# Optimization experiments

Hardware: AMD Instinct MI355X
Metric: run time of the kernel (lower is better)

The kernel has to match this reference:

```python
import jax, jax.numpy as jnp
import numpy as np

D_MODEL = 1024
D_STATE = 16
DT_RANK = 64
BATCH = 4
SEQ = 4096


def setup_inputs() -> dict:
    key = jax.random.key(0)
    ks = jax.random.split(key, 6)
    x = jax.random.normal(ks[0], (BATCH, SEQ, D_MODEL), dtype=jnp.float32)
    # torch nn.Linear weights: (out_features, in_features)
    W_xproj = jax.random.normal(ks[1], (DT_RANK + 2 * D_STATE, D_MODEL), dtype=jnp.float32) * (1.0 / np.sqrt(D_MODEL))
    W_dt = jax.random.normal(ks[2], (D_MODEL, DT_RANK), dtype=jnp.float32) * (1.0 / np.sqrt(DT_RANK))
    b_dt = jax.random.normal(ks[3], (D_MODEL,), dtype=jnp.float32) * 0.01
    A_log = jax.random.normal(ks[4], (D_MODEL, D_STATE), dtype=jnp.float32)
    D = jax.random.normal(ks[5], (D_MODEL,), dtype=jnp.float32)
    return {"x": x, "W_xproj": W_xproj, "W_dt": W_dt, "b_dt": b_dt, "A_log": A_log, "D": D}


def _selective_scan(x, delta, A, B, C):
    # x, delta: (b, s, d); B, C: (b, s, n); A: (d, n)
    b, s, d = x.shape
    n = A.shape[1]
    h0 = jnp.zeros((b, d, n), dtype=x.dtype)

    def step(h, inp):
        x_t, dt_t, B_t, C_t = inp  # (b,d), (b,d), (b,n), (b,n)
        dA = jnp.exp(dt_t[:, :, None] * A[None, :, :])        # (b,d,n)
        dB = dt_t[:, :, None] * B_t[:, None, :]               # (b,d,n)
        h = h * dA + x_t[:, :, None] * dB                     # (b,d,n)
        y_t = jnp.einsum('bdn,bn->bd', h, C_t)                # (b,d)
        return h, y_t

    # time-major for scan
    xs = (jnp.swapaxes(x, 0, 1), jnp.swapaxes(delta, 0, 1),
          jnp.swapaxes(B, 0, 1), jnp.swapaxes(C, 0, 1))
    _, ys = jax.lax.scan(step, h0, xs)  # ys: (s, b, d)
    return jnp.swapaxes(ys, 0, 1)


def reference(x, W_xproj, W_dt, b_dt, A_log, D):
    xp = jnp.einsum('bsd,pd->bsp', x, W_xproj)                # (b,s,dt_rank+2n)
    delta = jax.nn.softplus(jnp.einsum('bsr,dr->bsd', xp[..., :DT_RANK], W_dt) + b_dt)
    B = xp[..., DT_RANK:DT_RANK + D_STATE]
    C = xp[..., DT_RANK + D_STATE:]
    A = -jnp.exp(A_log)
    y = _selective_scan(x, delta, A, B, C)
    return y + x * D[None, None, :]
```

## Files before the change

### kernel.cpp

```cpp
#include <hip/hip_runtime.h>
#include <cstddef>

#define D_MODEL 1024
#define D_STATE 16
#define DT_RANK 64
#define BATCH 4
#define SEQ 4096
#define NPROJ 96
#define M_TOTAL (BATCH * SEQ)
#define NCHUNK 64
#define CLEN 64
#define KSPLIT 4
#define KSLICE 256

__device__ __forceinline__ float softplus_fast(float v) {
    return fmaxf(v, 0.0f) + __logf(1.0f + __expf(-fabsf(v)));
}

__global__ __launch_bounds__(256) void proj_part_kernel(const float* __restrict__ x,
                                                        const float* __restrict__ W,
                                                        float* __restrict__ part) {
    __shared__ float xs_t[32][68];
    __shared__ float ws_t[32][100];
    const int tid   = threadIdx.x;
    const int row0  = blockIdx.x * 64;
    const int ks    = blockIdx.y;
    const int kbase = ks * KSLICE;
    const int ty = tid >> 4;
    const int tx = tid & 15;

    float acc[4][6];
#pragma unroll
    for (int i = 0; i < 4; ++i)
#pragma unroll
        for (int j = 0; j < 6; ++j) acc[i][j] = 0.0f;

    for (int k0 = kbase; k0 < kbase + KSLICE; k0 += 32) {
        for (int i = tid; i < 64 * 8; i += 256) {
            int r = i >> 3, c4 = i & 7;
            float4 v = *reinterpret_cast<const float4*>(
                &x[(size_t)(row0 + r) * 1024 + k0 + c4 * 4]);
            xs_t[c4 * 4 + 0][r] = v.x; xs_t[c4 * 4 + 1][r] = v.y;
            xs_t[c4 * 4 + 2][r] = v.z; xs_t[c4 * 4 + 3][r] = v.w;
        }
        for (int i = tid; i < 96 * 8; i += 256) {
            int r = i >> 3, c4 = i & 7;
            float4 v = *reinterpret_cast<const float4*>(
                &W[(size_t)r * 1024 + k0 + c4 * 4]);
            ws_t[c4 * 4 + 0][r] = v.x; ws_t[c4 * 4 + 1][r] = v.y;
            ws_t[c4 * 4 + 2][r] = v.z; ws_t[c4 * 4 + 3][r] = v.w;
        }
        __syncthreads();
#pragma unroll 8
        for (int k = 0; k < 32; ++k) {
            float4 av = *reinterpret_cast<const float4*>(&xs_t[k][ty * 4]);
            float2 b0 = *reinterpret_cast<const float2*>(&ws_t[k][tx * 6]);
            float2 b1 = *reinterpret_cast<const float2*>(&ws_t[k][tx * 6 + 2]);
            float2 b2 = *reinterpret_cast<const float2*>(&ws_t[k][tx * 6 + 4]);
            float a[4] = {av.x, av.y, av.z, av.w};
            float b[6] = {b0.x, b0.y, b1.x, b1.y, b2.x, b2.y};
#pragma unroll
            for (int i = 0; i < 4; ++i)
#pragma unroll
                for (int j = 0; j < 6; ++j) acc[i][j] = fmaf(a[i], b[j], acc[i][j]);
        }
        __syncthreads();
    }
    size_t base = ((size_t)ks * M_TOTAL + row0) * NPROJ;
#pragma unroll
    for (int i = 0; i < 4; ++i) {
        size_t rbase = base + (size_t)(ty * 4 + i) * NPROJ + tx * 6;
#pragma unroll
        for (int j = 0; j < 6; ++j) part[rbase + j] = acc[i][j];
    }
}

__global__ __launch_bounds__(256) void reduce_xp_kernel(const float* __restrict__ part,
                                                        float* __restrict__ xp) {
    const size_t stride4 = (size_t)M_TOTAL * NPROJ / 4;
    size_t i = (size_t)blockIdx.x * 256 + threadIdx.x;
    const float4* p = reinterpret_cast<const float4*>(part);
    float4 a = p[i];
    float4 b = p[i + stride4];
    float4 c = p[i + 2 * stride4];
    float4 d = p[i + 3 * stride4];
    float4 o;
    o.x = (a.x + b.x) + (c.x + d.x);
    o.y = (a.y + b.y) + (c.y + d.y);
    o.z = (a.z + b.z) + (c.z + d.z);
    o.w = (a.w + b.w) + (c.w + d.w);
    reinterpret_cast<float4*>(xp)[i] = o;
}

__global__ __launch_bounds__(256) void delta_kernel(const float* __restrict__ xp,
                                                    const float* __restrict__ Wd,
                                                    const float* __restrict__ b_dt,
                                                    float* __restrict__ delta) {
    __shared__ float as_t[32][132];
    __shared__ float bs_t[32][132];
    const int tid  = threadIdx.x;
    const int row0 = blockIdx.x * 128;
    const int col0 = blockIdx.y * 128;
    const int ty = tid >> 4;
    const int tx = tid & 15;

    float acc[8][8];
#pragma unroll
    for (int i = 0; i < 8; ++i)
#pragma unroll
        for (int j = 0; j < 8; ++j) acc[i][j] = 0.0f;

    for (int k0 = 0; k0 < 64; k0 += 32) {
        for (int i = tid; i < 128 * 8; i += 256) {
            int r = i >> 3, c4 = i & 7;
            float4 v = *reinterpret_cast<const float4*>(
                &xp[(size_t)(row0 + r) * NPROJ + k0 + c4 * 4]);
            as_t[c4 * 4 + 0][r] = v.x; as_t[c4 * 4 + 1][r] = v.y;
            as_t[c4 * 4 + 2][r] = v.z; as_t[c4 * 4 + 3][r] = v.w;
        }
        for (int i = tid; i < 128 * 8; i += 256) {
            int r = i >> 3, c4 = i & 7;
            float4 v = *reinterpret_cast<const float4*>(
                &Wd[(size_t)(col0 + r) * 64 + k0 + c4 * 4]);
            bs_t[c4 * 4 + 0][r] = v.x; bs_t[c4 * 4 + 1][r] = v.y;
            bs_t[c4 * 4 + 2][r] = v.z; bs_t[c4 * 4 + 3][r] = v.w;
        }
        __syncthreads();
#pragma unroll 4
        for (int k = 0; k < 32; ++k) {
            float4 a0 = *reinterpret_cast<const float4*>(&as_t[k][ty * 8]);
            float4 a1 = *reinterpret_cast<const float4*>(&as_t[k][ty * 8 + 4]);
            float4 b0 = *reinterpret_cast<const float4*>(&bs_t[k][tx * 8]);
            float4 b1 = *reinterpret_cast<const float4*>(&bs_t[k][tx * 8 + 4]);
            float a[8] = {a0.x, a0.y, a0.z, a0.w, a1.x, a1.y, a1.z, a1.w};
            float b[8] = {b0.x, b0.y, b0.z, b0.w, b1.x, b1.y, b1.z, b1.w};
#pragma unroll
            for (int i = 0; i < 8; ++i)
#pragma unroll
                for (int j = 0; j < 8; ++j) acc[i][j] = fmaf(a[i], b[j], acc[i][j]);
        }
        __syncthreads();
    }

    float4 bias0 = *reinterpret_cast<const float4*>(&b_dt[col0 + tx * 8]);
    float4 bias1 = *reinterpret_cast<const float4*>(&b_dt[col0 + tx * 8 + 4]);
#pragma unroll
    for (int i = 0; i < 8; ++i) {
        int row = row0 + ty * 8 + i;
        float4 o0, o1;
        o0.x = softplus_fast(acc[i][0] + bias0.x);
        o0.y = softplus_fast(acc[i][1] + bias0.y);
        o0.z = softplus_fast(acc[i][2] + bias0.z);
        o0.w = softplus_fast(acc[i][3] + bias0.w);
        o1.x = softplus_fast(acc[i][4] + bias1.x);
        o1.y = softplus_fast(acc[i][5] + bias1.y);
        o1.z = softplus_fast(acc[i][6] + bias1.z);
        o1.w = softplus_fast(acc[i][7] + bias1.w);
        float* dst = &delta[(size_t)row * D_MODEL + col0 + tx * 8];
        *reinterpret_cast<float4*>(dst)     = o0;
        *reinterpret_cast<float4*>(dst + 4) = o1;
    }
}

__global__ __launch_bounds__(256) void scanA_kernel(const float* __restrict__ x,
                                                    const float* __restrict__ xp,
                                                    const float* __restrict__ delta,
                                                    const float* __restrict__ A_log,
                                                    float* __restrict__ P,
                                                    float* __restrict__ H) {
    const int chunk = blockIdx.x;
    const int b     = blockIdx.z;
    const int d     = blockIdx.y * 256 + threadIdx.x;

    float Av[16];
    const float4* Arow = reinterpret_cast<const float4*>(A_log + (size_t)d * D_STATE);
#pragma unroll
    for (int q = 0; q < 4; ++q) {
        float4 v = Arow[q];
        Av[q * 4 + 0] = -__expf(v.x); Av[q * 4 + 1] = -__expf(v.y);
        Av[q * 4 + 2] = -__expf(v.z); Av[q * 4 + 3] = -__expf(v.w);
    }
    float h[16];
#pragma unroll
    for (int n = 0; n < 16; ++n) h[n] = 0.0f;
    float sdv = 0.0f;

    const size_t m0 = (size_t)b * SEQ + (size_t)chunk * CLEN;
#pragma unroll 2
    for (int j = 0; j < CLEN; ++j) {
        size_t m = m0 + j;
        float dv = delta[m * D_MODEL + d];
        float xv = x[m * D_MODEL + d];
        float dtx = dv * xv;
        const float4* Bp = reinterpret_cast<const float4*>(xp + m * NPROJ + DT_RANK);
        float Bv[16];
        {
            float4 v0 = Bp[0], v1 = Bp[1], v2 = Bp[2], v3 = Bp[3];
            Bv[0]=v0.x; Bv[1]=v0.y; Bv[2]=v0.z; Bv[3]=v0.w;
            Bv[4]=v1.x; Bv[5]=v1.y; Bv[6]=v1.z; Bv[7]=v1.w;
            Bv[8]=v2.x; Bv[9]=v2.y; Bv[10]=v2.z; Bv[11]=v2.w;
            Bv[12]=v3.x; Bv[13]=v3.y; Bv[14]=v3.z; Bv[15]=v3.w;
        }
        sdv += dv;
#pragma unroll
        for (int n = 0; n < 16; ++n) {
            float a = __expf(dv * Av[n]);
            h[n] = fmaf(a, h[n], dtx * Bv[n]);
        }
    }
    size_t idx = (((size_t)chunk * BATCH + b) * D_MODEL + d) * D_STATE;
    float4* Pp = reinterpret_cast<float4*>(P + idx);
    float4* Hp = reinterpret_cast<float4*>(H + idx);
#pragma unroll
    for (int q = 0; q < 4; ++q) {
        float4 pv, hv;
        pv.x = __expf(Av[q*4+0] * sdv); pv.y = __expf(Av[q*4+1] * sdv);
        pv.z = __expf(Av[q*4+2] * sdv); pv.w = __expf(Av[q*4+3] * sdv);
        hv.x = h[q*4+0]; hv.y = h[q*4+1]; hv.z = h[q*4+2]; hv.w = h[q*4+3];
        Pp[q] = pv; Hp[q] = hv;
    }
}

__global__ __launch_bounds__(256) void scanB_kernel(float* __restrict__ P,
                                                    const float* __restrict__ H) {
    const int t = blockIdx.x * 256 + threadIdx.x;
    float carry = 0.0f;
    for (int c = 0; c < NCHUNK; ++c) {
        size_t idx = (size_t)c * (BATCH * D_MODEL * D_STATE) + t;
        float p  = P[idx];
        float hh = H[idx];
        P[idx] = carry;
        carry = fmaf(p, carry, hh);
    }
}

__global__ __launch_bounds__(256) void scanC_kernel(const float* __restrict__ x,
                                                    const float* __restrict__ xp,
                                                    const float* __restrict__ delta,
                                                    const float* __restrict__ A_log,
                                                    const float* __restrict__ Dvec,
                                                    const float* __restrict__ Hin,
                                                    float* __restrict__ out) {
    const int chunk = blockIdx.x;
    const int b     = blockIdx.z;
    const int d     = blockIdx.y * 256 + threadIdx.x;

    float Av[16];
    const float4* Arow = reinterpret_cast<const float4*>(A_log + (size_t)d * D_STATE);
#pragma unroll
    for (int q = 0; q < 4; ++q) {
        float4 v = Arow[q];
        Av[q * 4 + 0] = -__expf(v.x); Av[q * 4 + 1] = -__expf(v.y);
        Av[q * 4 + 2] = -__expf(v.z); Av[q * 4 + 3] = -__expf(v.w);
    }
    const float Dv = Dvec[d];

    float h[16];
    size_t idx = (((size_t)chunk * BATCH + b) * D_MODEL + d) * D_STATE;
    const float4* Hp = reinterpret_cast<const float4*>(Hin + idx);
#pragma unroll
    for (int q = 0; q < 4; ++q) {
        float4 v = Hp[q];
        h[q*4+0] = v.x; h[q*4+1] = v.y; h[q*4+2] = v.z; h[q*4+3] = v.w;
    }

    const size_t m0 = (size_t)b * SEQ + (size_t)chunk * CLEN;
#pragma unroll 2
    for (int j = 0; j < CLEN; ++j) {
        size_t m = m0 + j;
        float dv = delta[m * D_MODEL + d];
        float xv = x[m * D_MODEL + d];
        float dtx = dv * xv;
        const float4* Bp = reinterpret_cast<const float4*>(xp + m * NPROJ + DT_RANK);
        float Bv[16], Cv[16];
        {
            float4 v0 = Bp[0], v1 = Bp[1], v2 = Bp[2], v3 = Bp[3];
            Bv[0]=v0.x; Bv[1]=v0.y; Bv[2]=v0.z; Bv[3]=v0.w;
            Bv[4]=v1.x; Bv[5]=v1.y; Bv[6]=v1.z; Bv[7]=v1.w;
            Bv[8]=v2.x; Bv[9]=v2.y; Bv[10]=v2.z; Bv[11]=v2.w;
            Bv[12]=v3.x; Bv[13]=v3.y; Bv[14]=v3.z; Bv[15]=v3.w;
            float4 c0 = Bp[4], c1 = Bp[5], c2 = Bp[6], c3 = Bp[7];
            Cv[0]=c0.x; Cv[1]=c0.y; Cv[2]=c0.z; Cv[3]=c0.w;
            Cv[4]=c1.x; Cv[5]=c1.y; Cv[6]=c1.z; Cv[7]=c1.w;
            Cv[8]=c2.x; Cv[9]=c2.y; Cv[10]=c2.z; Cv[11]=c2.w;
            Cv[12]=c3.x; Cv[13]=c3.y; Cv[14]=c3.z; Cv[15]=c3.w;
        }
        float y = 0.0f;
#pragma unroll
        for (int n = 0; n < 16; ++n) {
            float a = __expf(dv * Av[n]);
            h[n] = fmaf(a, h[n], dtx * Bv[n]);
            y = fmaf(h[n], Cv[n], y);
        }
        out[m * D_MODEL + d] = fmaf(xv, Dv, y);
    }
}

extern "C" void kernel_launch(void* const* d_in, const int* in_sizes, int n_in,
                              void* d_out, int out_size, void* d_ws, size_t ws_size,
                              hipStream_t stream) {
    const float* x    = (const float*)d_in[0];
    const float* Wx   = (const float*)d_in[1];
    const float* Wd   = (const float*)d_in[2];
    const float* bdt  = (const float*)d_in[3];
    const float* Alog = (const float*)d_in[4];
    const float* Dv   = (const float*)d_in[5];
    float* out = (float*)d_out;

    float* ws    = (float*)d_ws;
    float* xp    = ws;
    float* delta = xp + (size_t)M_TOTAL * NPROJ;
    float* P     = delta + (size_t)M_TOTAL * D_MODEL;
    float* H     = P + (size_t)NCHUNK * BATCH * D_MODEL * D_STATE;
    float* part  = P;

    proj_part_kernel<<<dim3(M_TOTAL / 64, KSPLIT), 256, 0, stream>>>(x, Wx, part);
    reduce_xp_kernel<<<dim3((M_TOTAL * NPROJ / 4) / 256), 256, 0, stream>>>(part, xp);
    delta_kernel<<<dim3(M_TOTAL / 128, D_MODEL / 128), 256, 0, stream>>>(xp, Wd, bdt, delta);
    scanA_kernel<<<dim3(NCHUNK, D_MODEL / 256, BATCH), 256, 0, stream>>>(x, xp, delta, Alog, P, H);
    scanB_kernel<<<dim3((BATCH * D_MODEL * D_STATE) / 256), 256, 0, stream>>>(P, H);
    scanC_kernel<<<dim3(NCHUNK, D_MODEL / 256, BATCH), 256, 0, stream>>>(x, xp, delta, Alog, Dv, P, out);
}
```

Measured before the change: 317.1 us.

## Increase split-K and scan chunk parallelism, prefetch scan inputs, untranspose x tile

```diff
diff --git a/kernel.cpp b/kernel.cpp
--- a/kernel.cpp
+++ b/kernel.cpp
@@ -8,10 +8,6 @@
 #define SEQ 4096
 #define NPROJ 96
 #define M_TOTAL (BATCH * SEQ)
-#define NCHUNK 64
-#define CLEN 64
-#define KSPLIT 4
-#define KSLICE 256
 
 __device__ __forceinline__ float softplus_fast(float v) {
     return fmaxf(v, 0.0f) + __logf(1.0f + __expf(-fabsf(v)));
@@ -19,13 +15,13 @@
 
 __global__ __launch_bounds__(256) void proj_part_kernel(const float* __restrict__ x,
                                                         const float* __restrict__ W,
-                                                        float* __restrict__ part) {
-    __shared__ float xs_t[32][68];
+                                                        float* __restrict__ part,
+                                                        int kslice) {
+    __shared__ float xs[64][36];
     __shared__ float ws_t[32][100];
     const int tid   = threadIdx.x;
     const int row0  = blockIdx.x * 64;
-    const int ks    = blockIdx.y;
-    const int kbase = ks * KSLICE;
+    const int kbase = blockIdx.y * kslice;
     const int ty = tid >> 4;
     const int tx = tid & 15;
 
@@ -35,13 +31,12 @@
 #pragma unroll
         for (int j = 0; j < 6; ++j) acc[i][j] = 0.0f;
 
-    for (int k0 = kbase; k0 < kbase + KSLICE; k0 += 32) {
+    for (int k0 = kbase; k0 < kbase + kslice; k0 += 32) {
         for (int i = tid; i < 64 * 8; i += 256) {
             int r = i >> 3, c4 = i & 7;
             float4 v = *reinterpret_cast<const float4*>(
                 &x[(size_t)(row0 + r) * 1024 + k0 + c4 * 4]);
-            xs_t[c4 * 4 + 0][r] = v.x; xs_t[c4 * 4 + 1][r] = v.y;
-            xs_t[c4 * 4 + 2][r] = v.z; xs_t[c4 * 4 + 3][r] = v.w;
+            *reinterpret_cast<float4*>(&xs[r][c4 * 4]) = v;
         }
         for (int i = tid; i < 96 * 8; i += 256) {
             int r = i >> 3, c4 = i & 7;
@@ -53,11 +48,12 @@
         __syncthreads();
 #pragma unroll 8
         for (int k = 0; k < 32; ++k) {
-            float4 av = *reinterpret_cast<const float4*>(&xs_t[k][ty * 4]);
+            float a[4];
+#pragma unroll
+            for (int i = 0; i < 4; ++i) a[i] = xs[ty * 4 + i][k];
             float2 b0 = *reinterpret_cast<const float2*>(&ws_t[k][tx * 6]);
             float2 b1 = *reinterpret_cast<const float2*>(&ws_t[k][tx * 6 + 2]);
             float2 b2 = *reinterpret_cast<const float2*>(&ws_t[k][tx * 6 + 4]);
-            float a[4] = {av.x, av.y, av.z, av.w};
             float b[6] = {b0.x, b0.y, b1.x, b1.y, b2.x, b2.y};
 #pragma unroll
             for (int i = 0; i < 4; ++i)
@@ -66,7 +62,7 @@
         }
         __syncthreads();
     }
-    size_t base = ((size_t)ks * M_TOTAL + row0) * NPROJ;
+    size_t base = ((size_t)blockIdx.y * M_TOTAL + row0) * NPROJ;
 #pragma unroll
     for (int i = 0; i < 4; ++i) {
         size_t rbase = base + (size_t)(ty * 4 + i) * NPROJ + tx * 6;
@@ -76,20 +72,17 @@
 }
 
 __global__ __launch_bounds__(256) void reduce_xp_kernel(const float* __restrict__ part,
-                                                        float* __restrict__ xp) {
+                                                        float* __restrict__ xp,
+                                                        int ksplit) {
     const size_t stride4 = (size_t)M_TOTAL * NPROJ / 4;
     size_t i = (size_t)blockIdx.x * 256 + threadIdx.x;
     const float4* p = reinterpret_cast<const float4*>(part);
     float4 a = p[i];
-    float4 b = p[i + stride4];
-    float4 c = p[i + 2 * stride4];
-    float4 d = p[i + 3 * stride4];
-    float4 o;
-    o.x = (a.x + b.x) + (c.x + d.x);
-    o.y = (a.y + b.y) + (c.y + d.y);
-    o.z = (a.z + b.z) + (c.z + d.z);
-    o.w = (a.w + b.w) + (c.w + d.w);
-    reinterpret_cast<float4*>(xp)[i] = o;
+    for (int s = 1; s < ksplit; ++s) {
+        float4 b = p[i + (size_t)s * stride4];
+        a.x += b.x; a.y += b.y; a.z += b.z; a.w += b.w;
+    }
+    reinterpret_cast<float4*>(xp)[i] = a;
 }
 
 __global__ __launch_bounds__(256) void delta_kernel(const float* __restrict__ xp,
@@ -162,6 +155,7 @@
     }
 }
 
+template<int CLEN_T>
 __global__ __launch_bounds__(256) void scanA_kernel(const float* __restrict__ x,
                                                     const float* __restrict__ xp,
                                                     const float* __restrict__ delta,
@@ -177,36 +171,39 @@
 #pragma unroll
     for (int q = 0; q < 4; ++q) {
         float4 v = Arow[q];
-        Av[q * 4 + 0] = -__expf(v.x); Av[q * 4 + 1] = -__expf(v.y);
-        Av[q * 4 + 2] = -__expf(v.z); Av[q * 4 + 3] = -__expf(v.w);
+        Av[q*4+0] = -__expf(v.x); Av[q*4+1] = -__expf(v.y);
+        Av[q*4+2] = -__expf(v.z); Av[q*4+3] = -__expf(v.w);
     }
     float h[16];
 #pragma unroll
     for (int n = 0; n < 16; ++n) h[n] = 0.0f;
     float sdv = 0.0f;
 
-    const size_t m0 = (size_t)b * SEQ + (size_t)chunk * CLEN;
-#pragma unroll 2
-    for (int j = 0; j < CLEN; ++j) {
-        size_t m = m0 + j;
-        float dv = delta[m * D_MODEL + d];
-        float xv = x[m * D_MODEL + d];
-        float dtx = dv * xv;
-        const float4* Bp = reinterpret_cast<const float4*>(xp + m * NPROJ + DT_RANK);
-        float Bv[16];
-        {
-            float4 v0 = Bp[0], v1 = Bp[1], v2 = Bp[2], v3 = Bp[3];
-            Bv[0]=v0.x; Bv[1]=v0.y; Bv[2]=v0.z; Bv[3]=v0.w;
-            Bv[4]=v1.x; Bv[5]=v1.y; Bv[6]=v1.z; Bv[7]=v1.w;
-            Bv[8]=v2.x; Bv[9]=v2.y; Bv[10]=v2.z; Bv[11]=v2.w;
-            Bv[12]=v3.x; Bv[13]=v3.y; Bv[14]=v3.z; Bv[15]=v3.w;
-        }
-        sdv += dv;
+    const size_t m0 = (size_t)b * SEQ + (size_t)chunk * CLEN_T;
+    const size_t xbase = m0 * D_MODEL + d;
+    const size_t pbase = m0 * NPROJ + DT_RANK;
+
+    float dv_c = delta[xbase];
+    float xv_c = x[xbase];
+#pragma unroll 4
+    for (int j = 0; j < CLEN_T; ++j) {
+        float dv_n = 0.0f, xv_n = 0.0f;
+        if (j + 1 < CLEN_T) {
+            dv_n = delta[xbase + (size_t)(j + 1) * D_MODEL];
+            xv_n = x[xbase + (size_t)(j + 1) * D_MODEL];
+        }
+        const float4* Bp = reinterpret_cast<const float4*>(xp + pbase + (size_t)j * NPROJ);
+        float4 B0 = Bp[0], B1 = Bp[1], B2 = Bp[2], B3 = Bp[3];
+        float Bv[16] = {B0.x,B0.y,B0.z,B0.w, B1.x,B1.y,B1.z,B1.w,
+                        B2.x,B2.y,B2.z,B2.w, B3.x,B3.y,B3.z,B3.w};
+        float dtx = dv_c * xv_c;
+        sdv += dv_c;
 #pragma unroll
         for (int n = 0; n < 16; ++n) {
-            float a = __expf(dv * Av[n]);
+            float a = __expf(dv_c * Av[n]);
             h[n] = fmaf(a, h[n], dtx * Bv[n]);
         }
+        dv_c = dv_n; xv_c = xv_n;
     }
     size_t idx = (((size_t)chunk * BATCH + b) * D_MODEL + d) * D_STATE;
     float4* Pp = reinterpret_cast<float4*>(P + idx);
@@ -222,18 +219,25 @@
 }
 
 __global__ __launch_bounds__(256) void scanB_kernel(float* __restrict__ P,
-                                                    const float* __restrict__ H) {
+                                                    const float* __restrict__ H,
+                                                    int nchunk) {
     const int t = blockIdx.x * 256 + threadIdx.x;
+    const size_t cs = (size_t)BATCH * D_MODEL * D_STATE;
     float carry = 0.0f;
-    for (int c = 0; c < NCHUNK; ++c) {
-        size_t idx = (size_t)c * (BATCH * D_MODEL * D_STATE) + t;
-        float p  = P[idx];
-        float hh = H[idx];
-        P[idx] = carry;
-        carry = fmaf(p, carry, hh);
-    }
-}
-
+    float p_c = P[t], h_c = H[t];
+    for (int c = 0; c < nchunk; ++c) {
+        float p_n = 0.0f, h_n = 0.0f;
+        if (c + 1 < nchunk) {
+            p_n = P[(size_t)(c + 1) * cs + t];
+            h_n = H[(size_t)(c + 1) * cs + t];
+        }
+        P[(size_t)c * cs + t] = carry;
+        carry = fmaf(p_c, carry, h_c);
+        p_c = p_n; h_c = h_n;
+    }
+}
+
+template<int CLEN_T>
 __global__ __launch_bounds__(256) void scanC_kernel(const float* __restrict__ x,
                                                     const float* __restrict__ xp,
                                                     const float* __restrict__ delta,
@@ -250,8 +254,8 @@
 #pragma unroll
     for (int q = 0; q < 4; ++q) {
         float4 v = Arow[q];
-        Av[q * 4 + 0] = -__expf(v.x); Av[q * 4 + 1] = -__expf(v.y);
-        Av[q * 4 + 2] = -__expf(v.z); Av[q * 4 + 3] = -__expf(v.w);
+        Av[q*4+0] = -__expf(v.x); Av[q*4+1] = -__expf(v.y);
+        Av[q*4+2] = -__expf(v.z); Av[q*4+3] = -__expf(v.w);
     }
     const float Dv = Dvec[d];
 
@@ -264,35 +268,36 @@
         h[q*4+0] = v.x; h[q*4+1] = v.y; h[q*4+2] = v.z; h[q*4+3] = v.w;
     }
 
-    const size_t m0 = (size_t)b * SEQ + (size_t)chunk * CLEN;
-#pragma unroll 2
-    for (int j = 0; j < CLEN; ++j) {
-        size_t m = m0 + j;
-        float dv = delta[m * D_MODEL + d];
-        float xv = x[m * D_MODEL + d];
-        float dtx = dv * xv;
-        const float4* Bp = reinterpret_cast<const float4*>(xp + m * NPROJ + DT_RANK);
-        float Bv[16], Cv[16];
-        {
-            float4 v0 = Bp[0], v1 = Bp[1], v2 = Bp[2], v3 = Bp[3];
-            Bv[0]=v0.x; Bv[1]=v0.y; Bv[2]=v0.z; Bv[3]=v0.w;
-            Bv[4]=v1.x; Bv[5]=v1.y; Bv[6]=v1.z; Bv[7]=v1.w;
-            Bv[8]=v2.x; Bv[9]=v2.y; Bv[10]=v2.z; Bv[11]=v2.w;
-            Bv[12]=v3.x; Bv[13]=v3.y; Bv[14]=v3.z; Bv[15]=v3.w;
-            float4 c0 = Bp[4], c1 = Bp[5], c2 = Bp[6], c3 = Bp[7];
-            Cv[0]=c0.x; Cv[1]=c0.y; Cv[2]=c0.z; Cv[3]=c0.w;
-            Cv[4]=c1.x; Cv[5]=c1.y; Cv[6]=c1.z; Cv[7]=c1.w;
-            Cv[8]=c2.x; Cv[9]=c2.y; Cv[10]=c2.z; Cv[11]=c2.w;
-            Cv[12]=c3.x; Cv[13]=c3.y; Cv[14]=c3.z; Cv[15]=c3.w;
-        }
+    const size_t m0 = (size_t)b * SEQ + (size_t)chunk * CLEN_T;
+    const size_t xbase = m0 * D_MODEL + d;
+    const size_t pbase = m0 * NPROJ + DT_RANK;
+
+    float dv_c = delta[xbase];
+    float xv_c = x[xbase];
+#pragma unroll 4
+    for (int j = 0; j < CLEN_T; ++j) {
+        float dv_n = 0.0f, xv_n = 0.0f;
+        if (j + 1 < CLEN_T) {
+            dv_n = delta[xbase + (size_t)(j + 1) * D_MODEL];
+            xv_n = x[xbase + (size_t)(j + 1) * D_MODEL];
+        }
+        const float4* Bp = reinterpret_cast<const float4*>(xp + pbase + (size_t)j * NPROJ);
+        float4 B0 = Bp[0], B1 = Bp[1], B2 = Bp[2], B3 = Bp[3];
+        float4 C0 = Bp[4], C1 = Bp[5], C2 = Bp[6], C3 = Bp[7];
+        float Bv[16] = {B0.x,B0.y,B0.z,B0.w, B1.x,B1.y,B1.z,B1.w,
+                        B2.x,B2.y,B2.z,B2.w, B3.x,B3.y,B3.z,B3.w};
+        float Cv[16] = {C0.x,C0.y,C0.z,C0.w, C1.x,C1.y,C1.z,C1.w,
+                        C2.x,C2.y,C2.z,C2.w, C3.x,C3.y,C3.z,C3.w};
+        float dtx = dv_c * xv_c;
         float y = 0.0f;
 #pragma unroll
         for (int n = 0; n < 16; ++n) {
-            float a = __expf(dv * Av[n]);
+            float a = __expf(dv_c * Av[n]);
             h[n] = fmaf(a, h[n], dtx * Bv[n]);
             y = fmaf(h[n], Cv[n], y);
         }
-        out[m * D_MODEL + d] = fmaf(xv, Dv, y);
+        out[xbase + (size_t)j * D_MODEL] = fmaf(xv_c, Dv, y);
+        dv_c = dv_n; xv_c = xv_n;
     }
 }
 
@@ -310,14 +315,32 @@
     float* ws    = (float*)d_ws;
     float* xp    = ws;
     float* delta = xp + (size_t)M_TOTAL * NPROJ;
-    float* P     = delta + (size_t)M_TOTAL * D_MODEL;
-    float* H     = P + (size_t)NCHUNK * BATCH * D_MODEL * D_STATE;
-    float* part  = P;
-
-    proj_part_kernel<<<dim3(M_TOTAL / 64, KSPLIT), 256, 0, stream>>>(x, Wx, part);
-    reduce_xp_kernel<<<dim3((M_TOTAL * NPROJ / 4) / 256), 256, 0, stream>>>(part, xp);
+    float* scan0 = delta + (size_t)M_TOTAL * D_MODEL;
+    float* part  = scan0;
+
+    const size_t baseF = (size_t)M_TOTAL * NPROJ + (size_t)M_TOTAL * D_MODEL;
+    const size_t chunkF = (size_t)BATCH * D_MODEL * D_STATE;
+
+    int ksplit, nchunk;
+    size_t needA = (baseF + 2 * 128 * chunkF) * 4;
+    size_t needB = (baseF + (size_t)8 * M_TOTAL * NPROJ) * 4;
+    if (ws_size >= needA)      { ksplit = 8; nchunk = 128; }
+    else if (ws_size >= needB) { ksplit = 8; nchunk = 64;  }
+    else                       { ksplit = 4; nchunk = 64;  }
+
+    float* P = scan0;
+    float* H = scan0 + (size_t)nchunk * chunkF;
+
+    proj_part_kernel<<<dim3(M_TOTAL / 64, ksplit), 256, 0, stream>>>(x, Wx, part, 1024 / ksplit);
+    reduce_xp_kernel<<<dim3((M_TOTAL * NPROJ / 4) / 256), 256, 0, stream>>>(part, xp, ksplit);
     delta_kernel<<<dim3(M_TOTAL / 128, D_MODEL / 128), 256, 0, stream>>>(xp, Wd, bdt, delta);
-    scanA_kernel<<<dim3(NCHUNK, D_MODEL / 256, BATCH), 256, 0, stream>>>(x, xp, delta, Alog, P, H);
-    scanB_kernel<<<dim3((BATCH * D_MODEL * D_STATE) / 256), 256, 0, stream>>>(P, H);
-    scanC_kernel<<<dim3(NCHUNK, D_MODEL / 256, BATCH), 256, 0, stream>>>(x, xp, delta, Alog, Dv, P, out);
-}
+    if (nchunk == 128) {
+        scanA_kernel<32><<<dim3(128, 4, BATCH), 256, 0, stream>>>(x, xp, delta, Alog, P, H);
+        scanB_kernel<<<dim3(256), 256, 0, stream>>>(P, H, 128);
+        scanC_kernel<32><<<dim3(128, 4, BATCH), 256, 0, stream>>>(x, xp, delta, Alog, Dv, P, out);
+    } else {
+        scanA_kernel<64><<<dim3(64, 4, BATCH), 256, 0, stream>>>(x, xp, delta, Alog, P, H);
+        scanB_kernel<<<dim3(256), 256, 0, stream>>>(P, H, 64);
+        scanC_kernel<64><<<dim3(64, 4, BATCH), 256, 0, stream>>>(x, xp, delta, Alog, Dv, P, out);
+    }
+}
```

Result: slower. 349.4 us (+10.2%).

## Use split-bf16 MFMA for projection and delta GEMMs, exp2 in scans

Applied to the files above, without the earlier changes.

```diff
diff --git a/kernel.cpp b/kernel.cpp
--- a/kernel.cpp
+++ b/kernel.cpp
@@ -13,65 +13,92 @@
 #define KSPLIT 4
 #define KSLICE 256
 
+typedef __attribute__((ext_vector_type(8))) short bf16x8;
+typedef __attribute__((ext_vector_type(4))) short short4v;
+typedef __attribute__((ext_vector_type(4))) float f32x4;
+
 __device__ __forceinline__ float softplus_fast(float v) {
     return fmaxf(v, 0.0f) + __logf(1.0f + __expf(-fabsf(v)));
 }
 
-__global__ __launch_bounds__(256) void proj_part_kernel(const float* __restrict__ x,
+__device__ __forceinline__ short f2bf(float x) {
+    union { float f; unsigned u; } v; v.f = x;
+    unsigned r = (v.u + 0x7fffu + ((v.u >> 16) & 1u)) >> 16;
+    return (short)r;
+}
+__device__ __forceinline__ float bf2f(short s) {
+    union { unsigned u; float f; } v; v.u = ((unsigned)(unsigned short)s) << 16;
+    return v.f;
+}
+struct bfpair { short hi, lo; };
+__device__ __forceinline__ bfpair split_bf(float x) {
+    bfpair r;
+    r.hi = f2bf(x);
+    r.lo = f2bf(x - bf2f(r.hi));
+    return r;
+}
+__device__ __forceinline__ void split_bf4(float4 v, short4v& h, short4v& l) {
+    bfpair a = split_bf(v.x), b = split_bf(v.y), c = split_bf(v.z), d = split_bf(v.w);
+    h = (short4v){a.hi, b.hi, c.hi, d.hi};
+    l = (short4v){a.lo, b.lo, c.lo, d.lo};
+}
+
+__global__ __launch_bounds__(256) void proj_mfma_kernel(const float* __restrict__ x,
                                                         const float* __restrict__ W,
                                                         float* __restrict__ part) {
-    __shared__ float xs_t[32][68];
-    __shared__ float ws_t[32][100];
+    __shared__ short ah[64][40], al[64][40];
+    __shared__ short bh[96][40], bl[96][40];
     const int tid   = threadIdx.x;
     const int row0  = blockIdx.x * 64;
-    const int ks    = blockIdx.y;
-    const int kbase = ks * KSLICE;
-    const int ty = tid >> 4;
-    const int tx = tid & 15;
-
-    float acc[4][6];
-#pragma unroll
-    for (int i = 0; i < 4; ++i)
-#pragma unroll
-        for (int j = 0; j < 6; ++j) acc[i][j] = 0.0f;
+    const int kbase = blockIdx.y * KSLICE;
+    const int wid   = tid >> 6;
+    const int lane  = tid & 63;
+    const int l16   = lane & 15;
+    const int kg    = lane >> 4;
+
+    f32x4 acc[6];
+#pragma unroll
+    for (int c = 0; c < 6; ++c) acc[c] = (f32x4){0.f, 0.f, 0.f, 0.f};
 
     for (int k0 = kbase; k0 < kbase + KSLICE; k0 += 32) {
         for (int i = tid; i < 64 * 8; i += 256) {
             int r = i >> 3, c4 = i & 7;
             float4 v = *reinterpret_cast<const float4*>(
                 &x[(size_t)(row0 + r) * 1024 + k0 + c4 * 4]);
-            xs_t[c4 * 4 + 0][r] = v.x; xs_t[c4 * 4 + 1][r] = v.y;
-            xs_t[c4 * 4 + 2][r] = v.z; xs_t[c4 * 4 + 3][r] = v.w;
+            short4v h, l;
+            split_bf4(v, h, l);
+            *reinterpret_cast<short4v*>(&ah[r][c4 * 4]) = h;
+            *reinterpret_cast<short4v*>(&al[r][c4 * 4]) = l;
         }
         for (int i = tid; i < 96 * 8; i += 256) {
             int r = i >> 3, c4 = i & 7;
             float4 v = *reinterpret_cast<const float4*>(
                 &W[(size_t)r * 1024 + k0 + c4 * 4]);
-            ws_t[c4 * 4 + 0][r] = v.x; ws_t[c4 * 4 + 1][r] = v.y;
-            ws_t[c4 * 4 + 2][r] = v.z; ws_t[c4 * 4 + 3][r] = v.w;
+            short4v h, l;
+            split_bf4(v, h, l);
+            *reinterpret_cast<short4v*>(&bh[r][c4 * 4]) = h;
+            *reinterpret_cast<short4v*>(&bl[r][c4 * 4]) = l;
         }
         __syncthreads();
-#pragma unroll 8
-        for (int k = 0; k < 32; ++k) {
-            float4 av = *reinterpret_cast<const float4*>(&xs_t[k][ty * 4]);
-            float2 b0 = *reinterpret_cast<const float2*>(&ws_t[k][tx * 6]);
-            float2 b1 = *reinterpret_cast<const float2*>(&ws_t[k][tx * 6 + 2]);
-            float2 b2 = *reinterpret_cast<const float2*>(&ws_t[k][tx * 6 + 4]);
-            float a[4] = {av.x, av.y, av.z, av.w};
-            float b[6] = {b0.x, b0.y, b1.x, b1.y, b2.x, b2.y};
-#pragma unroll
-            for (int i = 0; i < 4; ++i)
-#pragma unroll
-                for (int j = 0; j < 6; ++j) acc[i][j] = fmaf(a[i], b[j], acc[i][j]);
+
+        bf16x8 a_h = *reinterpret_cast<const bf16x8*>(&ah[wid * 16 + l16][kg * 8]);
+        bf16x8 a_l = *reinterpret_cast<const bf16x8*>(&al[wid * 16 + l16][kg * 8]);
+#pragma unroll
+        for (int c = 0; c < 6; ++c) {
+            bf16x8 b_h = *reinterpret_cast<const bf16x8*>(&bh[c * 16 + l16][kg * 8]);
+            bf16x8 b_l = *reinterpret_cast<const bf16x8*>(&bl[c * 16 + l16][kg * 8]);
+            acc[c] = __builtin_amdgcn_mfma_f32_16x16x32_bf16(a_h, b_h, acc[c], 0, 0, 0);
+            acc[c] = __builtin_amdgcn_mfma_f32_16x16x32_bf16(a_h, b_l, acc[c], 0, 0, 0);
+            acc[c] = __builtin_amdgcn_mfma_f32_16x16x32_bf16(a_l, b_h, acc[c], 0, 0, 0);
         }
         __syncthreads();
     }
-    size_t base = ((size_t)ks * M_TOTAL + row0) * NPROJ;
-#pragma unroll
-    for (int i = 0; i < 4; ++i) {
-        size_t rbase = base + (size_t)(ty * 4 + i) * NPROJ + tx * 6;
-#pragma unroll
-        for (int j = 0; j < 6; ++j) part[rbase + j] = acc[i][j];
+    size_t base = ((size_t)blockIdx.y * M_TOTAL + row0 + wid * 16 + kg * 4) * NPROJ;
+#pragma unroll
+    for (int c = 0; c < 6; ++c) {
+#pragma unroll
+        for (int q = 0; q < 4; ++q)
+            part[base + (size_t)q * NPROJ + c * 16 + l16] = acc[c][q];
     }
 }
 
@@ -81,84 +108,75 @@
     size_t i = (size_t)blockIdx.x * 256 + threadIdx.x;
     const float4* p = reinterpret_cast<const float4*>(part);
     float4 a = p[i];
-    float4 b = p[i + stride4];
-    float4 c = p[i + 2 * stride4];
-    float4 d = p[i + 3 * stride4];
-    float4 o;
-    o.x = (a.x + b.x) + (c.x + d.x);
-    o.y = (a.y + b.y) + (c.y + d.y);
-    o.z = (a.z + b.z) + (c.z + d.z);
-    o.w = (a.w + b.w) + (c.w + d.w);
-    reinterpret_cast<float4*>(xp)[i] = o;
-}
-
-__global__ __launch_bounds__(256) void delta_kernel(const float* __restrict__ xp,
-                                                    const float* __restrict__ Wd,
-                                                    const float* __restrict__ b_dt,
-                                                    float* __restrict__ delta) {
-    __shared__ float as_t[32][132];
-    __shared__ float bs_t[32][132];
+#pragma unroll
+    for (int s = 1; s < KSPLIT; ++s) {
+        float4 b = p[i + (size_t)s * stride4];
+        a.x += b.x; a.y += b.y; a.z += b.z; a.w += b.w;
+    }
+    reinterpret_cast<float4*>(xp)[i] = a;
+}
+
+__global__ __launch_bounds__(256) void delta_mfma_kernel(const float* __restrict__ xp,
+                                                         const float* __restrict__ Wd,
+                                                         const float* __restrict__ b_dt,
+                                                         float* __restrict__ delta) {
+    __shared__ short ah[64][72], al[64][72];
+    __shared__ short bh[64][72], bl[64][72];
     const int tid  = threadIdx.x;
-    const int row0 = blockIdx.x * 128;
-    const int col0 = blockIdx.y * 128;
-    const int ty = tid >> 4;
-    const int tx = tid & 15;
-
-    float acc[8][8];
-#pragma unroll
-    for (int i = 0; i < 8; ++i)
-#pragma unroll
-        for (int j = 0; j < 8; ++j) acc[i][j] = 0.0f;
-
-    for (int k0 = 0; k0 < 64; k0 += 32) {
-        for (int i = tid; i < 128 * 8; i += 256) {
-            int r = i >> 3, c4 = i & 7;
-            float4 v = *reinterpret_cast<const float4*>(
-                &xp[(size_t)(row0 + r) * NPROJ + k0 + c4 * 4]);
-            as_t[c4 * 4 + 0][r] = v.x; as_t[c4 * 4 + 1][r] = v.y;
-            as_t[c4 * 4 + 2][r] = v.z; as_t[c4 * 4 + 3][r] = v.w;
-        }
-        for (int i = tid; i < 128 * 8; i += 256) {
-            int r = i >> 3, c4 = i & 7;
-            float4 v = *reinterpret_cast<const float4*>(
-                &Wd[(size_t)(col0 + r) * 64 + k0 + c4 * 4]);
-            bs_t[c4 * 4 + 0][r] = v.x; bs_t[c4 * 4 + 1][r] = v.y;
-            bs_t[c4 * 4 + 2][r] = v.z; bs_t[c4 * 4 + 3][r] = v.w;
-        }
-        __syncthreads();
-#pragma unroll 4
-        for (int k = 0; k < 32; ++k) {
-            float4 a0 = *reinterpret_cast<const float4*>(&as_t[k][ty * 8]);
-            float4 a1 = *reinterpret_cast<const float4*>(&as_t[k][ty * 8 + 4]);
-            float4 b0 = *reinterpret_cast<const float4*>(&bs_t[k][tx * 8]);
-            float4 b1 = *reinterpret_cast<const float4*>(&bs_t[k][tx * 8 + 4]);
-            float a[8] = {a0.x, a0.y, a0.z, a0.w, a1.x, a1.y, a1.z, a1.w};
-            float b[8] = {b0.x, b0.y, b0.z, b0.w, b1.x, b1.y, b1.z, b1.w};
-#pragma unroll
-            for (int i = 0; i < 8; ++i)
-#pragma unroll
-                for (int j = 0; j < 8; ++j) acc[i][j] = fmaf(a[i], b[j], acc[i][j]);
-        }
-        __syncthreads();
-    }
-
-    float4 bias0 = *reinterpret_cast<const float4*>(&b_dt[col0 + tx * 8]);
-    float4 bias1 = *reinterpret_cast<const float4*>(&b_dt[col0 + tx * 8 + 4]);
-#pragma unroll
-    for (int i = 0; i < 8; ++i) {
-        int row = row0 + ty * 8 + i;
-        float4 o0, o1;
-        o0.x = softplus_fast(acc[i][0] + bias0.x);
-        o0.y = softplus_fast(acc[i][1] + bias0.y);
-        o0.z = softplus_fast(acc[i][2] + bias0.z);
-        o0.w = softplus_fast(acc[i][3] + bias0.w);
-        o1.x = softplus_fast(acc[i][4] + bias1.x);
-        o1.y = softplus_fast(acc[i][5] + bias1.y);
-        o1.z = softplus_fast(acc[i][6] + bias1.z);
-        o1.w = softplus_fast(acc[i][7] + bias1.w);
-        float* dst = &delta[(size_t)row * D_MODEL + col0 + tx * 8];
-        *reinterpret_cast<float4*>(dst)     = o0;
-        *reinterpret_cast<float4*>(dst + 4) = o1;
+    const int row0 = blockIdx.x * 64;
+    const int col0 = blockIdx.y * 64;
+    const int wid  = tid >> 6;
+    const int lane = tid & 63;
+    const int l16  = lane & 15;
+    const int kg   = lane >> 4;
+
+    for (int i = tid; i < 64 * 16; i += 256) {
+        int r = i >> 4, c4 = i & 15;
+        float4 v = *reinterpret_cast<const float4*>(
+            &xp[(size_t)(row0 + r) * NPROJ + c4 * 4]);
+        short4v h, l;
+        split_bf4(v, h, l);
+        *reinterpret_cast<short4v*>(&ah[r][c4 * 4]) = h;
+        *reinterpret_cast<short4v*>(&al[r][c4 * 4]) = l;
+    }
+    for (int i = tid; i < 64 * 16; i += 256) {
+        int r = i >> 4, c4 = i & 15;
+        float4 v = *reinterpret_cast<const float4*>(
+            &Wd[(size_t)(col0 + r) * 64 + c4 * 4]);
+        short4v h, l;
+        split_bf4(v, h, l);
+        *reinterpret_cast<short4v*>(&bh[r][c4 * 4]) = h;
+        *reinterpret_cast<short4v*>(&bl[r][c4 * 4]) = l;
+    }
+    __syncthreads();
+
+    f32x4 acc[4];
+#pragma unroll
+    for (int j = 0; j < 4; ++j) acc[j] = (f32x4){0.f, 0.f, 0.f, 0.f};
+
+#pragma unroll
+    for (int ks = 0; ks < 2; ++ks) {
+        int koff = ks * 32 + kg * 8;
+        bf16x8 a_h = *reinterpret_cast<const bf16x8*>(&ah[wid * 16 + l16][koff]);
+        bf16x8 a_l = *reinterpret_cast<const bf16x8*>(&al[wid * 16 + l16][koff]);
+#pragma unroll
+        for (int j = 0; j < 4; ++j) {
+            bf16x8 b_h = *reinterpret_cast<const bf16x8*>(&bh[j * 16 + l16][koff]);
+            bf16x8 b_l = *reinterpret_cast<const bf16x8*>(&bl[j * 16 + l16][koff]);
+            acc[j] = __builtin_amdgcn_mfma_f32_16x16x32_bf16(a_h, b_h, acc[j], 0, 0, 0);
+            acc[j] = __builtin_amdgcn_mfma_f32_16x16x32_bf16(a_h, b_l, acc[j], 0, 0, 0);
+            acc[j] = __builtin_amdgcn_mfma_f32_16x16x32_bf16(a_l, b_h, acc[j], 0, 0, 0);
+        }
+    }
+
+    int row = row0 + wid * 16 + kg * 4;
+#pragma unroll
+    for (int j = 0; j < 4; ++j) {
+        int col = col0 + j * 16 + l16;
+        float bias = b_dt[col];
+#pragma unroll
+        for (int q = 0; q < 4; ++q)
+            delta[(size_t)(row + q) * D_MODEL + col] = softplus_fast(acc[j][q] + bias);
     }
 }
 
@@ -171,14 +189,15 @@
     const int chunk = blockIdx.x;
     const int b     = blockIdx.z;
     const int d     = blockIdx.y * 256 + threadIdx.x;
+    const float LOG2E = 1.4426950408889634f;
 
     float Av[16];
     const float4* Arow = reinterpret_cast<const float4*>(A_log + (size_t)d * D_STATE);
 #pragma unroll
     for (int q = 0; q < 4; ++q) {
         float4 v = Arow[q];
-        Av[q * 4 + 0] = -__expf(v.x); Av[q * 4 + 1] = -__expf(v.y);
-        Av[q * 4 + 2] = -__expf(v.z); Av[q * 4 + 3] = -__expf(v.w);
+        Av[q*4+0] = -__expf(v.x) * LOG2E; Av[q*4+1] = -__expf(v.y) * LOG2E;
+        Av[q*4+2] = -__expf(v.z) * LOG2E; Av[q*4+3] = -__expf(v.w) * LOG2E;
     }
     float h[16];
 #pragma unroll
@@ -186,25 +205,22 @@
     float sdv = 0.0f;
 
     const size_t m0 = (size_t)b * SEQ + (size_t)chunk * CLEN;
+    const size_t xbase = m0 * D_MODEL + d;
+    const size_t pbase = m0 * NPROJ + DT_RANK;
+
 #pragma unroll 2
     for (int j = 0; j < CLEN; ++j) {
-        size_t m = m0 + j;
-        float dv = delta[m * D_MODEL + d];
-        float xv = x[m * D_MODEL + d];
+        float dv = delta[xbase + (size_t)j * D_MODEL];
+        float xv = x[xbase + (size_t)j * D_MODEL];
         float dtx = dv * xv;
-        const float4* Bp = reinterpret_cast<const float4*>(xp + m * NPROJ + DT_RANK);
-        float Bv[16];
-        {
-            float4 v0 = Bp[0], v1 = Bp[1], v2 = Bp[2], v3 = Bp[3];
-            Bv[0]=v0.x; Bv[1]=v0.y; Bv[2]=v0.z; Bv[3]=v0.w;
-            Bv[4]=v1.x; Bv[5]=v1.y; Bv[6]=v1.z; Bv[7]=v1.w;
-            Bv[8]=v2.x; Bv[9]=v2.y; Bv[10]=v2.z; Bv[11]=v2.w;
-            Bv[12]=v3.x; Bv[13]=v3.y; Bv[14]=v3.z; Bv[15]=v3.w;
-        }
+        const float4* Bp = reinterpret_cast<const float4*>(xp + pbase + (size_t)j * NPROJ);
+        float4 B0 = Bp[0], B1 = Bp[1], B2 = Bp[2], B3 = Bp[3];
+        float Bv[16] = {B0.x,B0.y,B0.z,B0.w, B1.x,B1.y,B1.z,B1.w,
+                        B2.x,B2.y,B2.z,B2.w, B3.x,B3.y,B3.z,B3.w};
         sdv += dv;
 #pragma unroll
         for (int n = 0; n < 16; ++n) {
-            float a = __expf(dv * Av[n]);
+            float a = exp2f(dv * Av[n]);
             h[n] = fmaf(a, h[n], dtx * Bv[n]);
         }
     }
@@ -214,8 +230,8 @@
 #pragma unroll
     for (int q = 0; q < 4; ++q) {
         float4 pv, hv;
-        pv.x = __expf(Av[q*4+0] * sdv); pv.y = __expf(Av[q*4+1] * sdv);
-        pv.z = __expf(Av[q*4+2] * sdv); pv.w = __expf(Av[q*4+3] * sdv);
+        pv.x = exp2f(Av[q*4+0] * sdv); pv.y = exp2f(Av[q*4+1] * sdv);
+        pv.z = exp2f(Av[q*4+2] * sdv); pv.w = exp2f(Av[q*4+3] * sdv);
         hv.x = h[q*4+0]; hv.y = h[q*4+1]; hv.z = h[q*4+2]; hv.w = h[q*4+3];
         Pp[q] = pv; Hp[q] = hv;
     }
@@ -244,14 +260,15 @@
     const int chunk = blockIdx.x;
     const int b     = blockIdx.z;
     const int d     = blockIdx.y * 256 + threadIdx.x;
+    const float LOG2E = 1.4426950408889634f;
 
     float Av[16];
     const float4* Arow = reinterpret_cast<const float4*>(A_log + (size_t)d * D_STATE);
 #pragma unroll
     for (int q = 0; q < 4; ++q) {
         float4 v = Arow[q];
-        Av[q * 4 + 0] = -__expf(v.x); Av[q * 4 + 1] = -__expf(v.y);
-        Av[q * 4 + 2] = -__expf(v.z); Av[q * 4 + 3] = -__expf(v.w);
+        Av[q*4+0] = -__expf(v.x) * LOG2E; Av[q*4+1] = -__expf(v.y) * LOG2E;
+        Av[q*4+2] = -__expf(v.z) * LOG2E; Av[q*4+3] = -__expf(v.w) * LOG2E;
     }
     const float Dv = Dvec[d];
 
@@ -265,34 +282,29 @@
     }
 
     const size_t m0 = (size_t)b * SEQ + (size_t)chunk * CLEN;
+    const size_t xbase = m0 * D_MODEL + d;
+    const size_t pbase = m0 * NPROJ + DT_RANK;
+
 #pragma unroll 2
     for (int j = 0; j < CLEN; ++j) {
-        size_t m = m0 + j;
-        float dv = delta[m * D_MODEL + d];
-        float xv = x[m * D_MODEL + d];
+        float dv = delta[xbase + (size_t)j * D_MODEL];
+        float xv = x[xbase + (size_t)j * D_MODEL];
         float dtx = dv * xv;
-        const float4* Bp = reinterpret_cast<const float4*>(xp + m * NPROJ + DT_RANK);
-        float Bv[16], Cv[16];
-        {
-            float4 v0 = Bp[0], v1 = Bp[1], v2 = Bp[2], v3 = Bp[3];
-            Bv[0]=v0.x; Bv[1]=v0.y; Bv[2]=v0.z; Bv[3]=v0.w;
-            Bv[4]=v1.x; Bv[5]=v1.y; Bv[6]=v1.z; Bv[7]=v1.w;
-            Bv[8]=v2.x; Bv[9]=v2.y; Bv[10]=v2.z; Bv[11]=v2.w;
-            Bv[12]=v3.x; Bv[13]=v3.y; Bv[14]=v3.z; Bv[15]=v3.w;
-            float4 c0 = Bp[4], c1 = Bp[5], c2 = Bp[6], c3 = Bp[7];
-            Cv[0]=c0.x; Cv[1]=c0.y; Cv[2]=c0.z; Cv[3]=c0.w;
-            Cv[4]=c1.x; Cv[5]=c1.y; Cv[6]=c1.z; Cv[7]=c1.w;
-            Cv[8]=c2.x; Cv[9]=c2.y; Cv[10]=c2.z; Cv[11]=c2.w;
-            Cv[12]=c3.x; Cv[13]=c3.y; Cv[14]=c3.z; Cv[15]=c3.w;
-        }
+        const float4* Bp = reinterpret_cast<const float4*>(xp + pbase + (size_t)j * NPROJ);
+        float4 B0 = Bp[0], B1 = Bp[1], B2 = Bp[2], B3 = Bp[3];
+        float4 C0 = Bp[4], C1 = Bp[5], C2 = Bp[6], C3 = Bp[7];
+        float Bv[16] = {B0.x,B0.y,B0.z,B0.w, B1.x,B1.y,B1.z,B1.w,
+                        B2.x,B2.y,B2.z,B2.w, B3.x,B3.y,B3.z,B3.w};
+        float Cv[16] = {C0.x,C0.y,C0.z,C0.w, C1.x,C1.y,C1.z,C1.w,
+                        C2.x,C2.y,C2.z,C2.w, C3.x,C3.y,C3.z,C3.w};
         float y = 0.0f;
 #pragma unroll
         for (int n = 0; n < 16; ++n) {
-            float a = __expf(dv * Av[n]);
+            float a = exp2f(dv * Av[n]);
             h[n] = fmaf(a, h[n], dtx * Bv[n]);
             y = fmaf(h[n], Cv[n], y);
         }
-        out[m * D_MODEL + d] = fmaf(xv, Dv, y);
+        out[xbase + (size_t)j * D_MODEL] = fmaf(xv, Dv, y);
     }
 }
 
@@ -310,14 +322,15 @@
     float* ws    = (float*)d_ws;
     float* xp    = ws;
     float* delta = xp + (size_t)M_TOTAL * NPROJ;
-    float* P     = delta + (size_t)M_TOTAL * D_MODEL;
-    float* H     = P + (size_t)NCHUNK * BATCH * D_MODEL * D_STATE;
-    float* part  = P;
-
-    proj_part_kernel<<<dim3(M_TOTAL / 64, KSPLIT), 256, 0, stream>>>(x, Wx, part);
+    float* scan0 = delta + (size_t)M_TOTAL * D_MODEL;
+    float* part  = scan0;
+    float* P     = scan0;
+    float* H     = scan0 + (size_t)NCHUNK * BATCH * D_MODEL * D_STATE;
+
+    proj_mfma_kernel<<<dim3(M_TOTAL / 64, KSPLIT), 256, 0, stream>>>(x, Wx, part);
     reduce_xp_kernel<<<dim3((M_TOTAL * NPROJ / 4) / 256), 256, 0, stream>>>(part, xp);
-    delta_kernel<<<dim3(M_TOTAL / 128, D_MODEL / 128), 256, 0, stream>>>(xp, Wd, bdt, delta);
-    scanA_kernel<<<dim3(NCHUNK, D_MODEL / 256, BATCH), 256, 0, stream>>>(x, xp, delta, Alog, P, H);
+    delta_mfma_kernel<<<dim3(M_TOTAL / 64, D_MODEL / 64), 256, 0, stream>>>(xp, Wd, bdt, delta);
+    scanA_kernel<<<dim3(NCHUNK, 4, BATCH), 256, 0, stream>>>(x, xp, delta, Alog, P, H);
     scanB_kernel<<<dim3((BATCH * D_MODEL * D_STATE) / 256), 256, 0, stream>>>(P, H);
-    scanC_kernel<<<dim3(NCHUNK, D_MODEL / 256, BATCH), 256, 0, stream>>>(x, xp, delta, Alog, Dv, P, out);
-}
+    scanC_kernel<<<dim3(NCHUNK, 4, BATCH), 256, 0, stream>>>(x, xp, delta, Alog, Dv, P, out);
+}
```

Result: slower. 347.4 us (+9.5%).
